# Kernel tuning notes

Hardware: AMD Instinct MI355X
Metric: run time of the kernel (lower is better)

Reference implementation:

```python
import jax, jax.numpy as jnp
import numpy as np

N_NODES = 50000
N_EDGES = 800000
LEAKY_SLOPE = 0.25


def setup_inputs() -> dict:
    key = jax.random.key(0)
    ks = jax.random.split(key, 12)
    in_dim, h = 512, [256, 256, 128, 128]
    x = jax.random.normal(ks[0], (N_NODES, in_dim), dtype=jnp.float32)
    row = jax.random.randint(ks[1], (N_EDGES,), 0, N_NODES, dtype=jnp.int32)
    col = jax.random.randint(ks[2], (N_EDGES,), 0, N_NODES, dtype=jnp.int32)
    vals = jax.random.uniform(ks[3], (N_EDGES,), dtype=jnp.float32)
    def xavier(k, fan_in, fan_out):
        std = np.sqrt(2.0 / (fan_in + fan_out))
        return jax.random.normal(k, (fan_in, fan_out), dtype=jnp.float32) * std
    W1 = xavier(ks[4], in_dim, h[0]); b1 = jnp.zeros((h[0],), jnp.float32)
    W2 = xavier(ks[5], h[0], h[1]);  b2 = jnp.zeros((h[1],), jnp.float32)
    W3 = xavier(ks[6], h[1], h[2]);  b3 = jnp.zeros((h[2],), jnp.float32)
    W4 = xavier(ks[7], h[2], h[3]);  b4 = jnp.zeros((h[3],), jnp.float32)
    return {"x": x, "row": row, "col": col, "vals": vals,
            "W1": W1, "b1": b1, "W2": W2, "b2": b2,
            "W3": W3, "b3": b3, "W4": W4, "b4": b4}


def _gconv(x, row, col, vals, W, b):
    # support = x @ W  (dense transform), then SpMM: out[i] = sum_e vals[e] * support[col[e]] for row[e]==i
    support = x @ W
    msgs = support[col] * vals[:, None]           # [E, out_dim] gather + edge-weight
    out = jax.ops.segment_sum(msgs, row, num_segments=x.shape[0])  # scatter-add
    return out + b


def reference(x, row, col, vals, W1, b1, W2, b2, W3, b3, W4, b4):
    lrelu = lambda t: jnp.where(t >= 0, t, LEAKY_SLOPE * t)
    # dropout is identity in eval mode (deterministic reference)
    h = lrelu(_gconv(x, row, col, vals, W1, b1))
    h = lrelu(_gconv(h, row, col, vals, W2, b2))
    h = lrelu(_gconv(h, row, col, vals, W3, b3))
    h = lrelu(_gconv(h, row, col, vals, W4, b4))
    return h
```

## Files before the change

kernel.cpp:

```cpp
#include <hip/hip_runtime.h>
#include <hip/hip_bf16.h>

#define NN 50000
#define NE 800000
#define LEAKY 0.25f
#define SCAN_NB ((NN + 255) / 256)

typedef __attribute__((ext_vector_type(8))) short bf16x8;
typedef __attribute__((ext_vector_type(8))) ushort u16x8;
typedef __attribute__((ext_vector_type(4))) float f32x4;
typedef unsigned long long ull;

static __device__ __forceinline__ ushort f2bf(float f) {
    union { __hip_bfloat16 h; ushort u; } cv;
    cv.h = __float2bfloat16(f);
    return cv.u;
}
static __device__ __forceinline__ float bf2f(ushort u) {
    union { unsigned u; float f; } cv;
    cv.u = ((unsigned)u) << 16;
    return cv.f;
}

__global__ void cast_bf16_x8(const float4* __restrict__ in, u16x8* __restrict__ out, int n8) {
    int i = blockIdx.x * blockDim.x + threadIdx.x;
    if (i >= n8) return;
    float4 v0 = in[i * 2];
    float4 v1 = in[i * 2 + 1];
    u16x8 o;
    o[0] = f2bf(v0.x); o[1] = f2bf(v0.y); o[2] = f2bf(v0.z); o[3] = f2bf(v0.w);
    o[4] = f2bf(v1.x); o[5] = f2bf(v1.y); o[6] = f2bf(v1.z); o[7] = f2bf(v1.w);
    out[i] = o;
}

__global__ void cast_transpose_w(const float* __restrict__ W, ushort* __restrict__ Wt, int K, int N) {
    int idx = blockIdx.x * blockDim.x + threadIdx.x;
    if (idx >= K * N) return;
    int k = idx / N, n = idx % N;
    Wt[n * K + k] = f2bf(W[idx]);
}

__global__ __launch_bounds__(256) void gemm_bf16(
    const ushort* __restrict__ A, const ushort* __restrict__ Bt,
    ushort* __restrict__ C, int M, int N, int K)
{
    __shared__ ushort As[128 * 32];
    __shared__ ushort Bs[128 * 32];
    const int tid  = threadIdx.x;
    const int lane = tid & 63;
    const int wid  = tid >> 6;
    const int wr = wid >> 1, wc = wid & 1;
    const int m0 = blockIdx.x * 128;
    const int n0 = blockIdx.y * 128;

    int ar1 = m0 + (tid >> 2);      if (ar1 >= M) ar1 = M - 1;
    int ar2 = m0 + 64 + (tid >> 2); if (ar2 >= M) ar2 = M - 1;
    const int br1 = n0 + (tid >> 2);
    const int br2 = br1 + 64;
    const int ccol = (tid & 3) * 8;

    const ushort* gA1 = A + (size_t)ar1 * K + ccol;
    const ushort* gA2 = A + (size_t)ar2 * K + ccol;
    const ushort* gB1 = Bt + (size_t)br1 * K + ccol;
    const ushort* gB2 = Bt + (size_t)br2 * K + ccol;

    char* ldsA = (char*)As + wid * 1024;
    char* ldsB = (char*)Bs + wid * 1024;

    const int fr = lane & 15;
    const int fq = lane >> 4;

    const ushort* fragA = As + (wr * 64 + fr) * 32 + fq * 8;
    const ushort* fragB = Bs + (wc * 64 + fr) * 32 + fq * 8;

    f32x4 acc[4][4];
    #pragma unroll
    for (int i = 0; i < 4; ++i)
        #pragma unroll
        for (int j = 0; j < 4; ++j)
            acc[i][j] = {0.f, 0.f, 0.f, 0.f};

    for (int k0 = 0; k0 < K; k0 += 32) {
        __builtin_amdgcn_global_load_lds((const __attribute__((address_space(1))) void*)(gA1 + k0),
                                         (__attribute__((address_space(3))) void*)(ldsA), 16, 0, 0);
        __builtin_amdgcn_global_load_lds((const __attribute__((address_space(1))) void*)(gA2 + k0),
                                         (__attribute__((address_space(3))) void*)(ldsA + 4096), 16, 0, 0);
        __builtin_amdgcn_global_load_lds((const __attribute__((address_space(1))) void*)(gB1 + k0),
                                         (__attribute__((address_space(3))) void*)(ldsB), 16, 0, 0);
        __builtin_amdgcn_global_load_lds((const __attribute__((address_space(1))) void*)(gB2 + k0),
                                         (__attribute__((address_space(3))) void*)(ldsB + 4096), 16, 0, 0);
        __syncthreads();

        bf16x8 a[4], b[4];
        #pragma unroll
        for (int mi = 0; mi < 4; ++mi) a[mi] = *(const bf16x8*)(fragA + mi * 16 * 32);
        #pragma unroll
        for (int ni = 0; ni < 4; ++ni) b[ni] = *(const bf16x8*)(fragB + ni * 16 * 32);
        #pragma unroll
        for (int mi = 0; mi < 4; ++mi)
            #pragma unroll
            for (int ni = 0; ni < 4; ++ni)
                acc[mi][ni] = __builtin_amdgcn_mfma_f32_16x16x32_bf16(a[mi], b[ni], acc[mi][ni], 0, 0, 0);
        __syncthreads();
    }

    #pragma unroll
    for (int mi = 0; mi < 4; ++mi) {
        #pragma unroll
        for (int j = 0; j < 4; ++j) {
            int row = m0 + wr * 64 + mi * 16 + fq * 4 + j;
            if (row >= M) continue;
            #pragma unroll
            for (int ni = 0; ni < 4; ++ni) {
                int colg = n0 + wc * 64 + ni * 16 + fr;
                C[(size_t)row * N + colg] = f2bf(acc[mi][ni][j]);
            }
        }
    }
}

__global__ void hist_rows(const int* __restrict__ row, int* __restrict__ cnt) {
    int e = blockIdx.x * blockDim.x + threadIdx.x;
    if (e < NE) atomicAdd(&cnt[row[e]], 1);
}

__global__ void scan_bsum(const int* __restrict__ cnt, int* __restrict__ bsum) {
    int i = blockIdx.x * 256 + threadIdx.x;
    int v = (i < NN) ? cnt[i] : 0;
    #pragma unroll
    for (int off = 32; off >= 1; off >>= 1) v += __shfl_down(v, off);
    __shared__ int ws[4];
    if ((threadIdx.x & 63) == 0) ws[threadIdx.x >> 6] = v;
    __syncthreads();
    if (threadIdx.x == 0) bsum[blockIdx.x] = ws[0] + ws[1] + ws[2] + ws[3];
}

__global__ void scan_boff(const int* __restrict__ bsum, int* __restrict__ boff,
                          int* __restrict__ rowptr) {
    __shared__ int s[256];
    int t = threadIdx.x;
    int v = (t < SCAN_NB) ? bsum[t] : 0;
    s[t] = v;
    __syncthreads();
    #pragma unroll
    for (int off = 1; off < 256; off <<= 1) {
        int u = (t >= off) ? s[t - off] : 0;
        __syncthreads();
        s[t] += u;
        __syncthreads();
    }
    if (t < SCAN_NB) boff[t] = s[t] - v;
    if (t == 255) rowptr[NN] = s[255];
}

__global__ void scan_write(const int* __restrict__ cnt, const int* __restrict__ boff,
                           int* __restrict__ rowptr, int* __restrict__ rowcur) {
    __shared__ int s[256];
    int b = blockIdx.x;
    int t = threadIdx.x;
    int i = b * 256 + t;
    int v = (i < NN) ? cnt[i] : 0;
    s[t] = v;
    __syncthreads();
    #pragma unroll
    for (int off = 1; off < 256; off <<= 1) {
        int u = (t >= off) ? s[t - off] : 0;
        __syncthreads();
        s[t] += u;
        __syncthreads();
    }
    if (i < NN) {
        int ex = boff[b] + s[t] - v;
        rowptr[i] = ex;
        rowcur[i] = ex;
    }
}

__global__ void scatter_edges(const int* __restrict__ row, const int* __restrict__ col,
                              const float* __restrict__ vals,
                              int* __restrict__ rowcur,
                              ull* __restrict__ epack) {
    int e = blockIdx.x * blockDim.x + threadIdx.x;
    if (e < NE) {
        int p = atomicAdd(&rowcur[row[e]], 1);
        ull pk = ((ull)__float_as_uint(vals[e]) << 32) | (unsigned)col[e];
        epack[p] = pk;
    }
}

template<int DIM, bool OUT_BF16>
__global__ __launch_bounds__(256) void spmm_gather_bf16(
    const ushort* __restrict__ support,
    const int* __restrict__ rowptr,
    const ull* __restrict__ epack,
    const float* __restrict__ bias,
    void* __restrict__ out) {
    constexpr int LPR = DIM / 8;
    constexpr int RPB = 256 / LPR;
    int r = blockIdx.x * RPB + threadIdx.x / LPR;
    int lane = threadIdx.x % LPR;
    if (r >= NN) return;
    int s = rowptr[r], e = rowptr[r + 1];
    float acc0[8] = {}, acc1[8] = {};
    int i = s;
    for (; i + 3 < e; i += 4) {
        ull p0 = epack[i];
        ull p1 = epack[i + 1];
        ull p2 = epack[i + 2];
        ull p3 = epack[i + 3];
        const u16x8* a0 = (const u16x8*)(support + (size_t)(unsigned)p0 * DIM) + lane;
        const u16x8* a1 = (const u16x8*)(support + (size_t)(unsigned)p1 * DIM) + lane;
        const u16x8* a2 = (const u16x8*)(support + (size_t)(unsigned)p2 * DIM) + lane;
        const u16x8* a3 = (const u16x8*)(support + (size_t)(unsigned)p3 * DIM) + lane;
        u16x8 v0 = *a0;
        u16x8 v1 = *a1;
        u16x8 v2 = *a2;
        u16x8 v3 = *a3;
        float w0 = __uint_as_float((unsigned)(p0 >> 32));
        float w1 = __uint_as_float((unsigned)(p1 >> 32));
        float w2 = __uint_as_float((unsigned)(p2 >> 32));
        float w3 = __uint_as_float((unsigned)(p3 >> 32));
        #pragma unroll
        for (int j = 0; j < 8; ++j) acc0[j] += w0 * bf2f(v0[j]);
        #pragma unroll
        for (int j = 0; j < 8; ++j) acc1[j] += w1 * bf2f(v1[j]);
        #pragma unroll
        for (int j = 0; j < 8; ++j) acc0[j] += w2 * bf2f(v2[j]);
        #pragma unroll
        for (int j = 0; j < 8; ++j) acc1[j] += w3 * bf2f(v3[j]);
    }
    for (; i < e; ++i) {
        ull p0 = epack[i];
        float w0 = __uint_as_float((unsigned)(p0 >> 32));
        u16x8 v0 = *((const u16x8*)(support + (size_t)(unsigned)p0 * DIM) + lane);
        #pragma unroll
        for (int j = 0; j < 8; ++j) acc0[j] += w0 * bf2f(v0[j]);
    }
    const float4 bb0 = ((const float4*)bias)[lane * 2];
    const float4 bb1 = ((const float4*)bias)[lane * 2 + 1];
    float acc[8];
    #pragma unroll
    for (int j = 0; j < 8; ++j) acc[j] = acc0[j] + acc1[j];
    acc[0] += bb0.x; acc[1] += bb0.y; acc[2] += bb0.z; acc[3] += bb0.w;
    acc[4] += bb1.x; acc[5] += bb1.y; acc[6] += bb1.z; acc[7] += bb1.w;
    #pragma unroll
    for (int j = 0; j < 8; ++j) acc[j] = (acc[j] >= 0.f) ? acc[j] : LEAKY * acc[j];
    if (OUT_BF16) {
        ushort4 o0, o1;
        o0.x = f2bf(acc[0]); o0.y = f2bf(acc[1]); o0.z = f2bf(acc[2]); o0.w = f2bf(acc[3]);
        o1.x = f2bf(acc[4]); o1.y = f2bf(acc[5]); o1.z = f2bf(acc[6]); o1.w = f2bf(acc[7]);
        ((ushort4*)out)[(size_t)r * LPR * 2 + lane * 2]     = o0;
        ((ushort4*)out)[(size_t)r * LPR * 2 + lane * 2 + 1] = o1;
    } else {
        float4 f0 = {acc[0], acc[1], acc[2], acc[3]};
        float4 f1 = {acc[4], acc[5], acc[6], acc[7]};
        ((float4*)out)[(size_t)r * LPR * 2 + lane * 2]     = f0;
        ((float4*)out)[(size_t)r * LPR * 2 + lane * 2 + 1] = f1;
    }
}

extern "C" void kernel_launch(void* const* d_in, const int* in_sizes, int n_in,
                              void* d_out, int out_size, void* d_ws, size_t ws_size,
                              hipStream_t stream) {
    const float* x    = (const float*)d_in[0];
    const int*   row  = (const int*)d_in[1];
    const int*   col  = (const int*)d_in[2];
    const float* vals = (const float*)d_in[3];
    const float* W1 = (const float*)d_in[4];  const float* b1 = (const float*)d_in[5];
    const float* W2 = (const float*)d_in[6];  const float* b2 = (const float*)d_in[7];
    const float* W3 = (const float*)d_in[8];  const float* b3 = (const float*)d_in[9];
    const float* W4 = (const float*)d_in[10]; const float* b4 = (const float*)d_in[11];

    ushort* Xb = (ushort*)d_ws;
    ushort* Hb = Xb;
    ushort* S  = Xb + (size_t)NN * 512;
    ushort* Wt1 = S + (size_t)NN * 256;
    ushort* Wt2 = Wt1 + 512 * 256;
    ushort* Wt3 = Wt2 + 256 * 256;
    ushort* Wt4 = Wt3 + 256 * 128;
    int* cnt    = (int*)(Wt4 + 128 * 128);
    int* rowptr = cnt + NN;
    int* rowcur = rowptr + (NN + 1);
    int* pend   = rowcur + (NN + 1);
    ull* epack  = (ull*)pend;
    int* bsum   = (int*)(epack + NE);
    int* boff   = bsum + SCAN_NB;
    float* out  = (float*)d_out;

    {
        int n8 = NN * 512 / 8;
        cast_bf16_x8<<<(n8 + 255) / 256, 256, 0, stream>>>((const float4*)x, (u16x8*)Xb, n8);
        cast_transpose_w<<<(512 * 256 + 255) / 256, 256, 0, stream>>>(W1, Wt1, 512, 256);
        cast_transpose_w<<<(256 * 256 + 255) / 256, 256, 0, stream>>>(W2, Wt2, 256, 256);
        cast_transpose_w<<<(256 * 128 + 255) / 256, 256, 0, stream>>>(W3, Wt3, 256, 128);
        cast_transpose_w<<<(128 * 128 + 255) / 256, 256, 0, stream>>>(W4, Wt4, 128, 128);
    }

    hipMemsetAsync(cnt, 0, NN * sizeof(int), stream);
    hist_rows<<<(NE + 255) / 256, 256, 0, stream>>>(row, cnt);
    scan_bsum<<<SCAN_NB, 256, 0, stream>>>(cnt, bsum);
    scan_boff<<<1, 256, 0, stream>>>(bsum, boff, rowptr);
    scan_write<<<SCAN_NB, 256, 0, stream>>>(cnt, boff, rowptr, rowcur);
    scatter_edges<<<(NE + 255) / 256, 256, 0, stream>>>(row, col, vals, rowcur, epack);

    const int MT = (NN + 127) / 128;

    gemm_bf16<<<dim3(MT, 2), 256, 0, stream>>>(Xb, Wt1, S, NN, 256, 512);
    spmm_gather_bf16<256, true><<<(NN + 7) / 8, 256, 0, stream>>>(S, rowptr, epack, b1, Hb);
    gemm_bf16<<<dim3(MT, 2), 256, 0, stream>>>(Hb, Wt2, S, NN, 256, 256);
    spmm_gather_bf16<256, true><<<(NN + 7) / 8, 256, 0, stream>>>(S, rowptr, epack, b2, Hb);
    gemm_bf16<<<dim3(MT, 1), 256, 0, stream>>>(Hb, Wt3, S, NN, 128, 256);
    spmm_gather_bf16<128, true><<<(NN + 15) / 16, 256, 0, stream>>>(S, rowptr, epack, b3, Hb);
    gemm_bf16<<<dim3(MT, 1), 256, 0, stream>>>(Hb, Wt4, S, NN, 128, 128);
    spmm_gather_bf16<128, false><<<(NN + 15) / 16, 256, 0, stream>>>(S, rowptr, epack, b4, out);
}
```

Before: 377.1 us.

## Slice support features so each SpMM block gathers one L2-resident feature slice

The GEMM epilogue now writes the support matrix as 8 feature slices, each stored contiguously over all nodes. The SpMM kernel assigns one slice per block, taking the slice from the low bits of the block index, so each block gathers narrow rows from a much smaller array. The intent is to keep each slice's gathered data resident in a per-XCD L2 instead of doing random gathers over the full support matrix. The cost is re-reading the CSR edge list and row pointers once per slice, and issuing smaller gather transactions.

```diff
diff --git a/kernel.cpp b/kernel.cpp
--- a/kernel.cpp
+++ b/kernel.cpp
@@ -42,7 +42,7 @@
 
 __global__ __launch_bounds__(256) void gemm_bf16(
     const ushort* __restrict__ A, const ushort* __restrict__ Bt,
-    ushort* __restrict__ C, int M, int N, int K)
+    ushort* __restrict__ C, int M, int N, int K, int sf_log2)
 {
     __shared__ ushort As[128 * 32];
     __shared__ ushort Bs[128 * 32];
@@ -104,6 +104,7 @@
         __syncthreads();
     }
 
+    const int sf_mask = (1 << sf_log2) - 1;
     #pragma unroll
     for (int mi = 0; mi < 4; ++mi) {
         #pragma unroll
@@ -113,7 +114,9 @@
             #pragma unroll
             for (int ni = 0; ni < 4; ++ni) {
                 int colg = n0 + wc * 64 + ni * 16 + fr;
-                C[(size_t)row * N + colg] = f2bf(acc[mi][ni][j]);
+                int sl = colg >> sf_log2;
+                int off = colg & sf_mask;
+                C[(((size_t)sl * M + row) << sf_log2) + off] = f2bf(acc[mi][ni][j]);
             }
         }
     }
@@ -188,18 +191,21 @@
     }
 }
 
-template<int DIM, bool OUT_BF16>
-__global__ __launch_bounds__(256) void spmm_gather_bf16(
+template<int DIM, int SF, bool OUT_BF16>
+__global__ __launch_bounds__(256) void spmm_sliced(
     const ushort* __restrict__ support,
     const int* __restrict__ rowptr,
     const ull* __restrict__ epack,
     const float* __restrict__ bias,
     void* __restrict__ out) {
-    constexpr int LPR = DIM / 8;
-    constexpr int RPB = 256 / LPR;
-    int r = blockIdx.x * RPB + threadIdx.x / LPR;
-    int lane = threadIdx.x % LPR;
+    constexpr int LPS = SF / 8;
+    constexpr int RPB = 256 / LPS;
+    const int slice = blockIdx.x & 7;
+    const int rb    = blockIdx.x >> 3;
+    int r = rb * RPB + threadIdx.x / LPS;
+    int lane = threadIdx.x % LPS;
     if (r >= NN) return;
+    const ushort* sbase = support + ((size_t)slice * NN) * SF + lane * 8;
     int s = rowptr[r], e = rowptr[r + 1];
     float acc0[8] = {}, acc1[8] = {};
     int i = s;
@@ -208,14 +214,10 @@
         ull p1 = epack[i + 1];
         ull p2 = epack[i + 2];
         ull p3 = epack[i + 3];
-        const u16x8* a0 = (const u16x8*)(support + (size_t)(unsigned)p0 * DIM) + lane;
-        const u16x8* a1 = (const u16x8*)(support + (size_t)(unsigned)p1 * DIM) + lane;
-        const u16x8* a2 = (const u16x8*)(support + (size_t)(unsigned)p2 * DIM) + lane;
-        const u16x8* a3 = (const u16x8*)(support + (size_t)(unsigned)p3 * DIM) + lane;
-        u16x8 v0 = *a0;
-        u16x8 v1 = *a1;
-        u16x8 v2 = *a2;
-        u16x8 v3 = *a3;
+        u16x8 v0 = *(const u16x8*)(sbase + (size_t)(unsigned)p0 * SF);
+        u16x8 v1 = *(const u16x8*)(sbase + (size_t)(unsigned)p1 * SF);
+        u16x8 v2 = *(const u16x8*)(sbase + (size_t)(unsigned)p2 * SF);
+        u16x8 v3 = *(const u16x8*)(sbase + (size_t)(unsigned)p3 * SF);
         float w0 = __uint_as_float((unsigned)(p0 >> 32));
         float w1 = __uint_as_float((unsigned)(p1 >> 32));
         float w2 = __uint_as_float((unsigned)(p2 >> 32));
@@ -232,12 +234,13 @@
     for (; i < e; ++i) {
         ull p0 = epack[i];
         float w0 = __uint_as_float((unsigned)(p0 >> 32));
-        u16x8 v0 = *((const u16x8*)(support + (size_t)(unsigned)p0 * DIM) + lane);
+        u16x8 v0 = *(const u16x8*)(sbase + (size_t)(unsigned)p0 * SF);
         #pragma unroll
         for (int j = 0; j < 8; ++j) acc0[j] += w0 * bf2f(v0[j]);
     }
-    const float4 bb0 = ((const float4*)bias)[lane * 2];
-    const float4 bb1 = ((const float4*)bias)[lane * 2 + 1];
+    const int feat0 = slice * SF + lane * 8;
+    const float4 bb0 = *(const float4*)(bias + feat0);
+    const float4 bb1 = *(const float4*)(bias + feat0 + 4);
     float acc[8];
     #pragma unroll
     for (int j = 0; j < 8; ++j) acc[j] = acc0[j] + acc1[j];
@@ -249,13 +252,13 @@
         ushort4 o0, o1;
         o0.x = f2bf(acc[0]); o0.y = f2bf(acc[1]); o0.z = f2bf(acc[2]); o0.w = f2bf(acc[3]);
         o1.x = f2bf(acc[4]); o1.y = f2bf(acc[5]); o1.z = f2bf(acc[6]); o1.w = f2bf(acc[7]);
-        ((ushort4*)out)[(size_t)r * LPR * 2 + lane * 2]     = o0;
-        ((ushort4*)out)[(size_t)r * LPR * 2 + lane * 2 + 1] = o1;
+        ushort* op = (ushort*)out + (size_t)r * DIM + feat0;
+        *(ushort4*)op = o0;
+        *(ushort4*)(op + 4) = o1;
     } else {
-        float4 f0 = {acc[0], acc[1], acc[2], acc[3]};
-        float4 f1 = {acc[4], acc[5], acc[6], acc[7]};
-        ((float4*)out)[(size_t)r * LPR * 2 + lane * 2]     = f0;
-        ((float4*)out)[(size_t)r * LPR * 2 + lane * 2 + 1] = f1;
+        float* op = (float*)out + (size_t)r * DIM + feat0;
+        *(float4*)op = {acc[0], acc[1], acc[2], acc[3]};
+        *(float4*)(op + 4) = {acc[4], acc[5], acc[6], acc[7]};
     }
 }
 
@@ -304,13 +307,15 @@
     scatter_edges<<<(NE + 255) / 256, 256, 0, stream>>>(row, col, vals, rowcur, epack);
 
     const int MT = (NN + 127) / 128;
-
-    gemm_bf16<<<dim3(MT, 2), 256, 0, stream>>>(Xb, Wt1, S, NN, 256, 512);
-    spmm_gather_bf16<256, true><<<(NN + 7) / 8, 256, 0, stream>>>(S, rowptr, epack, b1, Hb);
-    gemm_bf16<<<dim3(MT, 2), 256, 0, stream>>>(Hb, Wt2, S, NN, 256, 256);
-    spmm_gather_bf16<256, true><<<(NN + 7) / 8, 256, 0, stream>>>(S, rowptr, epack, b2, Hb);
-    gemm_bf16<<<dim3(MT, 1), 256, 0, stream>>>(Hb, Wt3, S, NN, 128, 256);
-    spmm_gather_bf16<128, true><<<(NN + 15) / 16, 256, 0, stream>>>(S, rowptr, epack, b3, Hb);
-    gemm_bf16<<<dim3(MT, 1), 256, 0, stream>>>(Hb, Wt4, S, NN, 128, 128);
-    spmm_gather_bf16<128, false><<<(NN + 15) / 16, 256, 0, stream>>>(S, rowptr, epack, b4, out);
-}
+    const int G256 = ((NN + 63) / 64) * 8;
+    const int G128 = ((NN + 127) / 128) * 8;
+
+    gemm_bf16<<<dim3(MT, 2), 256, 0, stream>>>(Xb, Wt1, S, NN, 256, 512, 5);
+    spmm_sliced<256, 32, true><<<G256, 256, 0, stream>>>(S, rowptr, epack, b1, Hb);
+    gemm_bf16<<<dim3(MT, 2), 256, 0, stream>>>(Hb, Wt2, S, NN, 256, 256, 5);
+    spmm_sliced<256, 32, true><<<G256, 256, 0, stream>>>(S, rowptr, epack, b2, Hb);
+    gemm_bf16<<<dim3(MT, 1), 256, 0, stream>>>(Hb, Wt3, S, NN, 128, 256, 4);
+    spmm_sliced<128, 16, true><<<G128, 256, 0, stream>>>(S, rowptr, epack, b3, Hb);
+    gemm_bf16<<<dim3(MT, 1), 256, 0, stream>>>(Hb, Wt4, S, NN, 128, 128, 4);
+    spmm_sliced<128, 16, false><<<G128, 256, 0, stream>>>(S, rowptr, epack, b4, out);
+}
```

After: 431.0 us. 1.14x slower.
